# Kernel optimization log

Hardware: AMD Instinct MI355X
Metric: run time of the kernel (lower is better)

Reference implementation:

```python
import jax, jax.numpy as jnp
import numpy as np

SIZE = 1024
CODE_DIM = 256

def setup_inputs() -> dict:
    key = jax.random.key(0)
    k1, k2 = jax.random.split(key)
    z = jax.random.normal(k1, (32, CODE_DIM, 32, 32), dtype=jnp.float32)
    # nn.Embedding weight init: uniform(-1/size, 1/size)
    emb_weight = jax.random.uniform(k2, (SIZE, CODE_DIM), dtype=jnp.float32,
                                    minval=-1.0 / SIZE, maxval=1.0 / SIZE)
    return {"z": z, "emb_weight": emb_weight}

def reference(z, emb_weight):
    n, c, h, w = z.shape
    # [n, h, w, c] -> [n*h*w, c]
    z_ = jnp.transpose(z, (0, 2, 3, 1)).reshape(-1, c)
    # squared euclidean distances to all codes: ||z||^2 - 2 z.W^T + ||W||^2
    distances = (jnp.sum(z_ ** 2, axis=1, keepdims=True)
                 - 2.0 * jnp.matmul(z_, emb_weight.T)
                 + jnp.sum(emb_weight ** 2, axis=1)[None, :])
    encoding_indices = jnp.argmin(distances, axis=1).reshape(n, h, w)
    # gather codes and move channel back: [n, h, w, c] -> [n, c, h, w]
    quantized = jnp.transpose(emb_weight[encoding_indices], (0, 3, 1, 2))
    straight_through = jax.lax.stop_gradient(quantized - z) + z
    return (quantized, straight_through, encoding_indices)
```

## Files before the change

### kernel.cpp

```cpp
#include <hip/hip_runtime.h>
#include <cfloat>


#define P_TOTAL   32768
#define N_CODES   1024
#define Q_ELEMS   8388608
#define EPS_SCREEN 4.0e-3f
#define CAND_CAP  64

typedef __attribute__((ext_vector_type(8))) short bf16x8;
typedef __attribute__((ext_vector_type(4))) float f32x4;

#define GLOAD16(gsrc, ldst) \
  __builtin_amdgcn_global_load_lds((const __attribute__((address_space(1))) void*)(gsrc), \
                                   (__attribute__((address_space(3))) void*)(ldst), 16, 0, 0)

__device__ __forceinline__ unsigned short f2bf(float f) {
    unsigned u = __builtin_bit_cast(unsigned, f);
    u += 0x7FFF + ((u >> 16) & 1);
    return (unsigned short)(u >> 16);
}

__device__ __forceinline__ float sq_sep(float v) {
    float t = v * v;
    asm volatile("" : "+v"(t));
    return t;
}

__global__ void k0t_transpose(const float* __restrict__ wemb, float* __restrict__ wt) {
    __shared__ float tile[64 * 65];
    const int tid = threadIdx.x;
    const int ct = blockIdx.x >> 2, kt = blockIdx.x & 3;
    const int c0 = ct * 64, k0 = kt * 64;
    const int rr = tid >> 4, cg = tid & 15;
    #pragma unroll
    for (int i = 0; i < 4; ++i) {
        const int row = i * 16 + rr;
        const float4 v = *(const float4*)&wemb[(size_t)(c0 + row) * 256 + k0 + cg * 4];
        tile[row * 65 + cg * 4 + 0] = v.x;
        tile[row * 65 + cg * 4 + 1] = v.y;
        tile[row * 65 + cg * 4 + 2] = v.z;
        tile[row * 65 + cg * 4 + 3] = v.w;
    }
    __syncthreads();
    #pragma unroll
    for (int i = 0; i < 4; ++i) {
        const int krow = i * 16 + rr;
        float4 v;
        v.x = tile[(cg * 4 + 0) * 65 + krow];
        v.y = tile[(cg * 4 + 1) * 65 + krow];
        v.z = tile[(cg * 4 + 2) * 65 + krow];
        v.w = tile[(cg * 4 + 3) * 65 + krow];
        *(float4*)&wt[(size_t)(k0 + krow) * 1024 + c0 + cg * 4] = v;
    }
}

__global__ void k0w_pack(const float* __restrict__ wemb, unsigned short* __restrict__ whi) {
    const int t = blockIdx.x * 256 + threadIdx.x;
    const int c = t >> 5, g = t & 31;
    const float4 v0 = *(const float4*)&wemb[(size_t)c * 256 + g * 8];
    const float4 v1 = *(const float4*)&wemb[(size_t)c * 256 + g * 8 + 4];
    bf16x8 hv;
    hv[0] = (short)f2bf(v0.x); hv[1] = (short)f2bf(v0.y);
    hv[2] = (short)f2bf(v0.z); hv[3] = (short)f2bf(v0.w);
    hv[4] = (short)f2bf(v1.x); hv[5] = (short)f2bf(v1.y);
    hv[6] = (short)f2bf(v1.z); hv[7] = (short)f2bf(v1.w);
    const int gs = g ^ (c & 7);
    *(bf16x8*)(whi + (size_t)c * 256 + gs * 8) = hv;
}

#define T16S 280
__global__ void k0z_pack(const float* __restrict__ z, unsigned short* __restrict__ zhi) {
    __shared__ unsigned short t16[64 * T16S];
    const int tid = threadIdx.x;
    const int n = blockIdx.x >> 4, hc = blockIdx.x & 15;
    const int hw0 = hc * 64;
    const int w = tid >> 6, hl = tid & 63;
    #pragma unroll
    for (int i = 0; i < 64; ++i) {
        const int k = i * 4 + w;
        const float v = z[((size_t)(n * 256 + k) << 10) + hw0 + hl];
        t16[hl * T16S + k] = f2bf(v);
    }
    __syncthreads();
    const int row = tid >> 2, cp = tid & 3;
    const size_t p0 = (size_t)(n * 1024 + hw0);
    #pragma unroll
    for (int i = 0; i < 8; ++i) {
        const int chunk = i * 4 + cp;
        *(bf16x8*)(zhi + (p0 + row) * 256 + chunk * 8) =
            *(const bf16x8*)&t16[row * T16S + chunk * 8];
    }
}

__global__ void k1_wsq(const float* __restrict__ wemb, float* __restrict__ wsq,
                       int* __restrict__ candCnt) {
    const int b = blockIdx.x, tid = threadIdx.x;
    if (b >= 4) { candCnt[(b - 4) * 256 + tid] = 0; return; }
    const int c = b * 256 + tid;
    const float* base = wemb + (size_t)c * 256;
    float half[2];
    #pragma unroll
    for (int h = 0; h < 2; ++h) {
        const float* x = base + h * 128;
        float r[8];
        #pragma unroll
        for (int j = 0; j < 8; ++j) r[j] = sq_sep(x[j]);
        for (int i = 8; i < 128; i += 8) {
            #pragma unroll
            for (int j = 0; j < 8; ++j) r[j] += sq_sep(x[i + j]);
        }
        half[h] = ((r[0] + r[1]) + (r[2] + r[3])) + ((r[4] + r[5]) + (r[6] + r[7]));
    }
    wsq[c] = half[0] + half[1];
}

__launch_bounds__(256, 4)
__global__ void k2s_screen(const unsigned short* __restrict__ zhi,
                           const unsigned short* __restrict__ whi,
                           const float* __restrict__ wsq,
                           unsigned short* __restrict__ candC,
                           float* __restrict__ candD,
                           int* __restrict__ candCnt) {
    __shared__ unsigned short Bs[2][32 * 256];
    __shared__ float wsqs[512];
    const int tid = threadIdx.x, bid = blockIdx.x;
    const int pgrp = bid >> 1, half = bid & 1;
    const int w = tid >> 6, l = tid & 63;
    const int la = l & 15, kg = l >> 4;
    const int m0 = pgrp * 64 + w * 16;
    const int cb0 = half * 512;

    wsqs[tid]       = wsq[cb0 + tid];
    wsqs[tid + 256] = wsq[cb0 + tid + 256];

    bf16x8 af[8];
    #pragma unroll
    for (int ks = 0; ks < 8; ++ks)
        af[ks] = *(const bf16x8*)(zhi + (size_t)(m0 + la) * 256 + ks * 32 + kg * 8);

    float rg[4];
    #pragma unroll
    for (int r = 0; r < 4; ++r) rg[r] = FLT_MAX;

#define STAGEB(buf, cb_) do {                                                  \
    const unsigned short* src_ = whi + (size_t)(cb_) * 256;                    \
    _Pragma("unroll")                                                          \
    for (int i_ = 0; i_ < 4; ++i_)                                             \
        GLOAD16(src_ + i_ * 2048 + tid * 8, &Bs[buf][i_ * 2048 + tid * 8]);    \
} while (0)

    STAGEB(0, cb0);
    __syncthreads();

    for (int ch = 0; ch < 16; ++ch) {
        const int cur = ch & 1;
        const int cb = cb0 + ch * 32;
        if (ch < 15) STAGEB(cur ^ 1, cb + 32);

        float wsqv[2];
        #pragma unroll
        for (int nf = 0; nf < 2; ++nf) wsqv[nf] = wsqs[ch * 32 + nf * 16 + la];

        f32x4 acc[2];
        #pragma unroll
        for (int nf = 0; nf < 2; ++nf) acc[nf] = (f32x4){0.f, 0.f, 0.f, 0.f};

        #pragma unroll
        for (int ks = 0; ks < 8; ++ks) {
            bf16x8 bfv[2];
            #pragma unroll
            for (int nf = 0; nf < 2; ++nf) {
                const int cl = nf * 16 + la;
                const int slot = (ks * 4 + kg) ^ (cl & 7);
                bfv[nf] = *(const bf16x8*)&Bs[cur][cl * 256 + slot * 8];
            }
            #pragma unroll
            for (int nf = 0; nf < 2; ++nf)
                acc[nf] = __builtin_amdgcn_mfma_f32_16x16x32_bf16(
                    af[ks], bfv[nf], acc[nf], 0, 0, 0);
        }

        float da[2][4];
        #pragma unroll
        for (int nf = 0; nf < 2; ++nf)
            #pragma unroll
            for (int r = 0; r < 4; ++r)
                da[nf][r] = __builtin_fmaf(-2.f, acc[nf][r], wsqv[nf]);

        bool need = false;
        #pragma unroll
        for (int r = 0; r < 4; ++r) {
            float mv = fminf(da[0][r], da[1][r]);
            #pragma unroll
            for (int off = 1; off < 16; off <<= 1)
                mv = fminf(mv, __shfl_xor(mv, off));
            need = need || (mv <= rg[r] + EPS_SCREEN);
            rg[r] = fminf(rg[r], mv);
        }

        if (need) {
            #pragma unroll
            for (int nf = 0; nf < 2; ++nf)
                #pragma unroll
                for (int r = 0; r < 4; ++r)
                    if (da[nf][r] <= rg[r] + EPS_SCREEN) {
                        const int p = m0 + kg * 4 + r;
                        const int slot = atomicAdd(&candCnt[p], 1);
                        if (slot < CAND_CAP) {
                            candC[(size_t)p * CAND_CAP + slot] =
                                (unsigned short)(cb + nf * 16 + la);
                            candD[(size_t)p * CAND_CAP + slot] = da[nf][r];
                        }
                    }
        }

        __syncthreads();
    }
#undef STAGEB
}

__launch_bounds__(256, 4)
__global__ void k2r_rescore(const float* __restrict__ z, const float* __restrict__ wemb,
                            const float* __restrict__ wsq,
                            const unsigned short* __restrict__ candC,
                            const float* __restrict__ candD,
                            const int* __restrict__ candCnt,
                            float* __restrict__ idx_out) {
    __shared__ float t32[32 * 256];
    const int tid = threadIdx.x;
    const int wv = tid >> 6, l = tid & 63;
    const int p0 = blockIdx.x * 32;
    const int n = p0 >> 10, hw0 = p0 & 1023;

    const int pl = tid >> 3, slot = tid & 7;
    const int p = p0 + pl;
    const int count = candCnt[p];
    const int c0raw = candC[(size_t)p * CAND_CAP + slot];
    const float da0 = candD[(size_t)p * CAND_CAP + slot];

    const int row = l & 31;
    const int xmr = (row & 7) * 4;
    #pragma unroll
    for (int i = 0; i < 8; ++i) {
        const int k4 = i * 32 + wv * 8 + (l >> 5) * 4;
        const size_t zb = ((size_t)(n * 256 + k4) << 10) + hw0 + row;
        float4 v;
        v.x = z[zb];
        v.y = z[zb + 1024];
        v.z = z[zb + 2048];
        v.w = z[zb + 3072];
        *(float4*)&t32[row * 256 + (k4 ^ xmr)] = v;
    }

    bool need;
    float thr = 0.f;
    if (count <= CAND_CAP) {
        const int nr = (count + 7) >> 3;
        float m = (slot < count) ? da0 : FLT_MAX;
        for (int rr = 1; rr < nr; ++rr) {
            const int s = rr * 8 + slot;
            if (s < count) m = fminf(m, candD[(size_t)p * CAND_CAP + s]);
        }
        #pragma unroll
        for (int off = 1; off < 8; off <<= 1) m = fminf(m, __shfl_xor(m, off));
        thr = m + EPS_SCREEN;

        int V;
        int soleC = N_CODES;
        {
            const bool v0 = (slot < count) && (da0 <= thr);
            const unsigned long long mask = __ballot(v0);
            V = __popcll((mask >> ((l >> 3) * 8)) & 0xFFull);
            if (v0) soleC = c0raw;
        }
        for (int rr = 1; rr < nr; ++rr) {
            const int s = rr * 8 + slot;
            bool vs = false;
            if (s < count) {
                vs = (candD[(size_t)p * CAND_CAP + s] <= thr);
                if (vs && soleC == N_CODES) soleC = candC[(size_t)p * CAND_CAP + s];
            }
            const unsigned long long mask = __ballot(vs);
            V += __popcll((mask >> ((l >> 3) * 8)) & 0xFFull);
        }
        if (V == 1 && soleC != N_CODES) idx_out[p] = (float)soleC;
        need = (V >= 2);
    } else {
        need = true;
    }

    __syncthreads();

    if (!need) return;

    const float* zrow = &t32[pl * 256];
    const int xm = (pl & 7) * 4;

    float halfv[2];
    #pragma unroll
    for (int h = 0; h < 2; ++h) {
        float r[8];
        {
            const f32x4 a = *(const f32x4*)&zrow[(h * 128) ^ xm];
            const f32x4 b = *(const f32x4*)&zrow[(h * 128 + 4) ^ xm];
            #pragma unroll
            for (int j = 0; j < 4; ++j) { r[j] = sq_sep(a[j]); r[4 + j] = sq_sep(b[j]); }
        }
        for (int i = 8; i < 128; i += 8) {
            const f32x4 a = *(const f32x4*)&zrow[(h * 128 + i) ^ xm];
            const f32x4 b = *(const f32x4*)&zrow[(h * 128 + i + 4) ^ xm];
            #pragma unroll
            for (int j = 0; j < 4; ++j) { r[j] += sq_sep(a[j]); r[4 + j] += sq_sep(b[j]); }
        }
        halfv[h] = ((r[0] + r[1]) + (r[2] + r[3])) + ((r[4] + r[5]) + (r[6] + r[7]));
    }
    const float zsv = halfv[0] + halfv[1];

#define DOT_CHAIN(wb_, dot_) do {                                              \
    _Pragma("unroll")                                                          \
    for (int kb = 0; kb < 256; kb += 8) {                                      \
        const f32x4 za = *(const f32x4*)&zrow[kb ^ xm];                        \
        const f32x4 zb4 = *(const f32x4*)&zrow[(kb + 4) ^ xm];                 \
        const float4 wa = *(const float4*)&(wb_)[kb];                          \
        const float4 wc = *(const float4*)&(wb_)[kb + 4];                      \
        dot_ = __builtin_fmaf(za[0], wa.x, dot_);                              \
        dot_ = __builtin_fmaf(za[1], wa.y, dot_);                              \
        dot_ = __builtin_fmaf(za[2], wa.z, dot_);                              \
        dot_ = __builtin_fmaf(za[3], wa.w, dot_);                              \
        dot_ = __builtin_fmaf(zb4[0], wc.x, dot_);                             \
        dot_ = __builtin_fmaf(zb4[1], wc.y, dot_);                             \
        dot_ = __builtin_fmaf(zb4[2], wc.z, dot_);                             \
        dot_ = __builtin_fmaf(zb4[3], wc.w, dot_);                             \
    }                                                                          \
} while (0)

    float bd = FLT_MAX;
    int bc = N_CODES;

    if (count <= CAND_CAP) {
        const int nr = (count + 7) >> 3;
        for (int rr = 0; rr < nr; ++rr) {
            const int s = rr * 8 + slot;
            int c; float das;
            if (rr == 0) { c = c0raw; das = da0; }
            else if (s < count) {
                c = candC[(size_t)p * CAND_CAP + s];
                das = candD[(size_t)p * CAND_CAP + s];
            } else { c = N_CODES; das = FLT_MAX; }
            if (s < count && das <= thr) {
                const float* wb = wemb + (size_t)c * 256;
                float dot = 0.f;
                DOT_CHAIN(wb, dot);
                const float d = __builtin_fmaf(-2.f, dot, zsv) + wsq[c];
                if (d < bd || (d == bd && c < bc)) { bd = d; bc = c; }
            }
        }
    } else {
        for (int rr = 0; rr < 128; ++rr) {
            const int c = rr * 8 + slot;
            const float* wb = wemb + (size_t)c * 256;
            float dot = 0.f;
            DOT_CHAIN(wb, dot);
            const float d = __builtin_fmaf(-2.f, dot, zsv) + wsq[c];
            if (d < bd || (d == bd && c < bc)) { bd = d; bc = c; }
        }
    }
#undef DOT_CHAIN

    #pragma unroll
    for (int off = 1; off < 8; off <<= 1) {
        const float od = __shfl_xor(bd, off);
        const int   oi = __shfl_xor(bc, off);
        if (od < bd || (od == bd && oi < bc)) { bd = od; bc = oi; }
    }
    if (slot == 0) idx_out[p] = (float)bc;
}

__global__ void k3_gather(const float* __restrict__ z, const float* __restrict__ wtf,
                          const float* __restrict__ idxf,
                          float* __restrict__ out0, float* __restrict__ out1) {
    __shared__ float wcol[1024];
    const int tid = threadIdx.x;
    const int b = blockIdx.x;
    const int c = b & 255, n = b >> 8;
    *(float4*)&wcol[tid * 4] = *(const float4*)&wtf[(size_t)c * 1024 + tid * 4];
    __syncthreads();

    const size_t zo = (((size_t)(n * 256 + c)) << 10) + tid * 4;
    const float4 zv = *(const float4*)&z[zo];
    const float4 iv = *(const float4*)&idxf[n * 1024 + tid * 4];
    float4 qv, st;
    qv.x = wcol[(int)iv.x]; st.x = (qv.x - zv.x) + zv.x;
    qv.y = wcol[(int)iv.y]; st.y = (qv.y - zv.y) + zv.y;
    qv.z = wcol[(int)iv.z]; st.z = (qv.z - zv.z) + zv.z;
    qv.w = wcol[(int)iv.w]; st.w = (qv.w - zv.w) + zv.w;
    *(float4*)&out0[zo] = qv;
    *(float4*)&out1[zo] = st;
}

extern "C" void kernel_launch(void* const* d_in, const int* in_sizes, int n_in,
                              void* d_out, int out_size, void* d_ws, size_t ws_size,
                              hipStream_t stream) {
    const float* z = (const float*)d_in[0];
    const float* wemb = (const float*)d_in[1];
    float* out = (float*)d_out;
    float* out0 = out;
    float* out1 = out + Q_ELEMS;
    float* oidx = out + 2 * Q_ELEMS;
    unsigned short* zhi = (unsigned short*)out0;
    unsigned short* candC = (unsigned short*)(out0 + 4194304);
    float* candD = out0 + 5242880;
    int* candCnt = (int*)(out0 + 7340032);
    unsigned short* whi = (unsigned short*)out1;
    float* wsq = (float*)d_ws;
    float* wtf = (float*)d_ws + 1024;

    k0t_transpose<<<64, 256, 0, stream>>>(wemb, wtf);
    k0w_pack<<<128, 256, 0, stream>>>(wemb, whi);
    k0z_pack<<<512, 256, 0, stream>>>(z, zhi);
    k1_wsq<<<132, 256, 0, stream>>>(wemb, wsq, candCnt);
    k2s_screen<<<1024, 256, 0, stream>>>(zhi, whi, wsq, candC, candD, candCnt);
    k2r_rescore<<<P_TOTAL / 32, 256, 0, stream>>>(z, wemb, wsq, candC, candD, candCnt, oidx);
    k3_gather<<<8192, 256, 0, stream>>>(z, wtf, oidx, out0, out1);
}
```

Before: 171.1 us.

## Split screening kernel across codebook quarters with smaller code chunks

The screening kernel now divides the codebook into four quarters of 256 codes instead of two halves of 512, and launches twice as many blocks. Each chunk covers 16 codes, so each wave issues one MFMA per k-step instead of two. Block indices are remapped so consecutive blocks share a codebook quarter, which should help L2 reuse. The min-occupancy launch bound is dropped. The aim is more parallelism and lower per-block LDS use. In exchange, each query's A fragments are loaded more times, there is less MFMA ILP per chunk, and more candidates may be emitted, since each quarter starts its running minimum fresh.

```diff
diff --git a/kernel.cpp b/kernel.cpp
--- a/kernel.cpp
+++ b/kernel.cpp
@@ -115,24 +115,24 @@
     wsq[c] = half[0] + half[1];
 }
 
-__launch_bounds__(256, 4)
+__launch_bounds__(256)
 __global__ void k2s_screen(const unsigned short* __restrict__ zhi,
                            const unsigned short* __restrict__ whi,
                            const float* __restrict__ wsq,
                            unsigned short* __restrict__ candC,
                            float* __restrict__ candD,
                            int* __restrict__ candCnt) {
-    __shared__ unsigned short Bs[2][32 * 256];
-    __shared__ float wsqs[512];
+    __shared__ unsigned short Bs[2][16 * 256];
+    __shared__ float wsqs[256];
     const int tid = threadIdx.x, bid = blockIdx.x;
-    const int pgrp = bid >> 1, half = bid & 1;
+    const int pgrp = (bid & 7) | ((bid >> 5) << 3);
+    const int q = (bid >> 3) & 3;
     const int w = tid >> 6, l = tid & 63;
     const int la = l & 15, kg = l >> 4;
     const int m0 = pgrp * 64 + w * 16;
-    const int cb0 = half * 512;
-
-    wsqs[tid]       = wsq[cb0 + tid];
-    wsqs[tid + 256] = wsq[cb0 + tid + 256];
+    const int cb0 = q * 256;
+
+    wsqs[tid] = wsq[cb0 + tid];
 
     bf16x8 af[8];
     #pragma unroll
@@ -146,7 +146,7 @@
 #define STAGEB(buf, cb_) do {                                                  \
     const unsigned short* src_ = whi + (size_t)(cb_) * 256;                    \
     _Pragma("unroll")                                                          \
-    for (int i_ = 0; i_ < 4; ++i_)                                             \
+    for (int i_ = 0; i_ < 2; ++i_)                                             \
         GLOAD16(src_ + i_ * 2048 + tid * 8, &Bs[buf][i_ * 2048 + tid * 8]);    \
 } while (0)
 
@@ -155,43 +155,28 @@
 
     for (int ch = 0; ch < 16; ++ch) {
         const int cur = ch & 1;
-        const int cb = cb0 + ch * 32;
-        if (ch < 15) STAGEB(cur ^ 1, cb + 32);
-
-        float wsqv[2];
-        #pragma unroll
-        for (int nf = 0; nf < 2; ++nf) wsqv[nf] = wsqs[ch * 32 + nf * 16 + la];
-
-        f32x4 acc[2];
-        #pragma unroll
-        for (int nf = 0; nf < 2; ++nf) acc[nf] = (f32x4){0.f, 0.f, 0.f, 0.f};
-
+        const int cb = cb0 + ch * 16;
+        if (ch < 15) STAGEB(cur ^ 1, cb + 16);
+
+        const float wsqv = wsqs[ch * 16 + la];
+
+        f32x4 acc = (f32x4){0.f, 0.f, 0.f, 0.f};
         #pragma unroll
         for (int ks = 0; ks < 8; ++ks) {
-            bf16x8 bfv[2];
-            #pragma unroll
-            for (int nf = 0; nf < 2; ++nf) {
-                const int cl = nf * 16 + la;
-                const int slot = (ks * 4 + kg) ^ (cl & 7);
-                bfv[nf] = *(const bf16x8*)&Bs[cur][cl * 256 + slot * 8];
-            }
-            #pragma unroll
-            for (int nf = 0; nf < 2; ++nf)
-                acc[nf] = __builtin_amdgcn_mfma_f32_16x16x32_bf16(
-                    af[ks], bfv[nf], acc[nf], 0, 0, 0);
-        }
-
-        float da[2][4];
+            const int slot = (ks * 4 + kg) ^ (la & 7);
+            const bf16x8 bf = *(const bf16x8*)&Bs[cur][la * 256 + slot * 8];
+            acc = __builtin_amdgcn_mfma_f32_16x16x32_bf16(af[ks], bf, acc, 0, 0, 0);
+        }
+
+        float da[4];
         #pragma unroll
-        for (int nf = 0; nf < 2; ++nf)
-            #pragma unroll
-            for (int r = 0; r < 4; ++r)
-                da[nf][r] = __builtin_fmaf(-2.f, acc[nf][r], wsqv[nf]);
+        for (int r = 0; r < 4; ++r)
+            da[r] = __builtin_fmaf(-2.f, acc[r], wsqv);
 
         bool need = false;
         #pragma unroll
         for (int r = 0; r < 4; ++r) {
-            float mv = fminf(da[0][r], da[1][r]);
+            float mv = da[r];
             #pragma unroll
             for (int off = 1; off < 16; off <<= 1)
                 mv = fminf(mv, __shfl_xor(mv, off));
@@ -201,18 +186,16 @@
 
         if (need) {
             #pragma unroll
-            for (int nf = 0; nf < 2; ++nf)
-                #pragma unroll
-                for (int r = 0; r < 4; ++r)
-                    if (da[nf][r] <= rg[r] + EPS_SCREEN) {
-                        const int p = m0 + kg * 4 + r;
-                        const int slot = atomicAdd(&candCnt[p], 1);
-                        if (slot < CAND_CAP) {
-                            candC[(size_t)p * CAND_CAP + slot] =
-                                (unsigned short)(cb + nf * 16 + la);
-                            candD[(size_t)p * CAND_CAP + slot] = da[nf][r];
-                        }
+            for (int r = 0; r < 4; ++r)
+                if (da[r] <= rg[r] + EPS_SCREEN) {
+                    const int p = m0 + kg * 4 + r;
+                    const int slot = atomicAdd(&candCnt[p], 1);
+                    if (slot < CAND_CAP) {
+                        candC[(size_t)p * CAND_CAP + slot] =
+                            (unsigned short)(cb + la);
+                        candD[(size_t)p * CAND_CAP + slot] = da[r];
                     }
+                }
         }
 
         __syncthreads();
@@ -420,7 +403,7 @@
     k0w_pack<<<128, 256, 0, stream>>>(wemb, whi);
     k0z_pack<<<512, 256, 0, stream>>>(z, zhi);
     k1_wsq<<<132, 256, 0, stream>>>(wemb, wsq, candCnt);
-    k2s_screen<<<1024, 256, 0, stream>>>(zhi, whi, wsq, candC, candD, candCnt);
+    k2s_screen<<<2048, 256, 0, stream>>>(zhi, whi, wsq, candC, candD, candCnt);
     k2r_rescore<<<P_TOTAL / 32, 256, 0, stream>>>(z, wemb, wsq, candC, candD, candCnt, oidx);
     k3_gather<<<8192, 256, 0, stream>>>(z, wtf, oidx, out0, out1);
 }
```

Measured after the change: 203.3 us. 18.8% more time.

## Load codebook fragments directly from global memory in screening kernel

Applied to the files above, without the earlier changes.

The screening kernel no longer stages bf16 codebook chunks into double-buffered LDS through global_load_lds. Each lane now reads its B fragments straight from global memory (served by L1/L2), so the swizzled packing, the per-chunk barrier and the wave-uniform 'need' pre-check are dropped, and launch_bounds no longer pins occupancy. This removes LDS traffic and synchronisation but makes every wave re-fetch the codebook from cache with scattered 16-byte loads, and without LDS prefetch the global-load latency is exposed.

```diff
diff --git a/kernel.cpp b/kernel.cpp
--- a/kernel.cpp
+++ b/kernel.cpp
@@ -10,10 +10,6 @@
 
 typedef __attribute__((ext_vector_type(8))) short bf16x8;
 typedef __attribute__((ext_vector_type(4))) float f32x4;
-
-#define GLOAD16(gsrc, ldst) \
-  __builtin_amdgcn_global_load_lds((const __attribute__((address_space(1))) void*)(gsrc), \
-                                   (__attribute__((address_space(3))) void*)(ldst), 16, 0, 0)
 
 __device__ __forceinline__ unsigned short f2bf(float f) {
     unsigned u = __builtin_bit_cast(unsigned, f);
@@ -65,8 +61,7 @@
     hv[2] = (short)f2bf(v0.z); hv[3] = (short)f2bf(v0.w);
     hv[4] = (short)f2bf(v1.x); hv[5] = (short)f2bf(v1.y);
     hv[6] = (short)f2bf(v1.z); hv[7] = (short)f2bf(v1.w);
-    const int gs = g ^ (c & 7);
-    *(bf16x8*)(whi + (size_t)c * 256 + gs * 8) = hv;
+    *(bf16x8*)(whi + (size_t)c * 256 + g * 8) = hv;
 }
 
 #define T16S 280
@@ -115,14 +110,13 @@
     wsq[c] = half[0] + half[1];
 }
 
-__launch_bounds__(256, 4)
+__launch_bounds__(256)
 __global__ void k2s_screen(const unsigned short* __restrict__ zhi,
                            const unsigned short* __restrict__ whi,
                            const float* __restrict__ wsq,
                            unsigned short* __restrict__ candC,
                            float* __restrict__ candD,
                            int* __restrict__ candCnt) {
-    __shared__ unsigned short Bs[2][32 * 256];
     __shared__ float wsqs[512];
     const int tid = threadIdx.x, bid = blockIdx.x;
     const int pgrp = bid >> 1, half = bid & 1;
@@ -143,42 +137,28 @@
     #pragma unroll
     for (int r = 0; r < 4; ++r) rg[r] = FLT_MAX;
 
-#define STAGEB(buf, cb_) do {                                                  \
-    const unsigned short* src_ = whi + (size_t)(cb_) * 256;                    \
-    _Pragma("unroll")                                                          \
-    for (int i_ = 0; i_ < 4; ++i_)                                             \
-        GLOAD16(src_ + i_ * 2048 + tid * 8, &Bs[buf][i_ * 2048 + tid * 8]);    \
-} while (0)
-
-    STAGEB(0, cb0);
-    __syncthreads();
+    __syncthreads();
+
+    const unsigned short* wbase = whi + ((size_t)(cb0 + la) << 8) + kg * 8;
 
     for (int ch = 0; ch < 16; ++ch) {
-        const int cur = ch & 1;
         const int cb = cb0 + ch * 32;
-        if (ch < 15) STAGEB(cur ^ 1, cb + 32);
+        const unsigned short* wrow = wbase + (size_t)ch * 32 * 256;
 
         float wsqv[2];
-        #pragma unroll
-        for (int nf = 0; nf < 2; ++nf) wsqv[nf] = wsqs[ch * 32 + nf * 16 + la];
+        wsqv[0] = wsqs[ch * 32 + la];
+        wsqv[1] = wsqs[ch * 32 + 16 + la];
 
         f32x4 acc[2];
-        #pragma unroll
-        for (int nf = 0; nf < 2; ++nf) acc[nf] = (f32x4){0.f, 0.f, 0.f, 0.f};
+        acc[0] = (f32x4){0.f, 0.f, 0.f, 0.f};
+        acc[1] = (f32x4){0.f, 0.f, 0.f, 0.f};
 
         #pragma unroll
         for (int ks = 0; ks < 8; ++ks) {
-            bf16x8 bfv[2];
-            #pragma unroll
-            for (int nf = 0; nf < 2; ++nf) {
-                const int cl = nf * 16 + la;
-                const int slot = (ks * 4 + kg) ^ (cl & 7);
-                bfv[nf] = *(const bf16x8*)&Bs[cur][cl * 256 + slot * 8];
-            }
-            #pragma unroll
-            for (int nf = 0; nf < 2; ++nf)
-                acc[nf] = __builtin_amdgcn_mfma_f32_16x16x32_bf16(
-                    af[ks], bfv[nf], acc[nf], 0, 0, 0);
+            const bf16x8 b0 = *(const bf16x8*)(wrow + ks * 32);
+            const bf16x8 b1 = *(const bf16x8*)(wrow + 4096 + ks * 32);
+            acc[0] = __builtin_amdgcn_mfma_f32_16x16x32_bf16(af[ks], b0, acc[0], 0, 0, 0);
+            acc[1] = __builtin_amdgcn_mfma_f32_16x16x32_bf16(af[ks], b1, acc[1], 0, 0, 0);
         }
 
         float da[2][4];
@@ -188,36 +168,29 @@
             for (int r = 0; r < 4; ++r)
                 da[nf][r] = __builtin_fmaf(-2.f, acc[nf][r], wsqv[nf]);
 
-        bool need = false;
         #pragma unroll
         for (int r = 0; r < 4; ++r) {
             float mv = fminf(da[0][r], da[1][r]);
             #pragma unroll
             for (int off = 1; off < 16; off <<= 1)
                 mv = fminf(mv, __shfl_xor(mv, off));
-            need = need || (mv <= rg[r] + EPS_SCREEN);
             rg[r] = fminf(rg[r], mv);
         }
 
-        if (need) {
-            #pragma unroll
-            for (int nf = 0; nf < 2; ++nf)
-                #pragma unroll
-                for (int r = 0; r < 4; ++r)
-                    if (da[nf][r] <= rg[r] + EPS_SCREEN) {
-                        const int p = m0 + kg * 4 + r;
-                        const int slot = atomicAdd(&candCnt[p], 1);
-                        if (slot < CAND_CAP) {
-                            candC[(size_t)p * CAND_CAP + slot] =
-                                (unsigned short)(cb + nf * 16 + la);
-                            candD[(size_t)p * CAND_CAP + slot] = da[nf][r];
-                        }
+        #pragma unroll
+        for (int nf = 0; nf < 2; ++nf)
+            #pragma unroll
+            for (int r = 0; r < 4; ++r)
+                if (da[nf][r] <= rg[r] + EPS_SCREEN) {
+                    const int p = m0 + kg * 4 + r;
+                    const int slot = atomicAdd(&candCnt[p], 1);
+                    if (slot < CAND_CAP) {
+                        candC[(size_t)p * CAND_CAP + slot] =
+                            (unsigned short)(cb + nf * 16 + la);
+                        candD[(size_t)p * CAND_CAP + slot] = da[nf][r];
                     }
-        }
-
-        __syncthreads();
-    }
-#undef STAGEB
+                }
+    }
 }
 
 __launch_bounds__(256, 4)
```

Result: slower. 238.4 us (+39.3%).
